# Optimization experiments

Hardware: AMD Instinct MI355X
Metric: run time of the kernel (lower is better)

Reference implementation:

```python
import jax, jax.numpy as jnp
import numpy as np
import math

NUM_HEADS = 16
ATTN_WIDTH = 256


def setup_inputs() -> dict:
    key = jax.random.key(0)
    ks = jax.random.split(key, 5)
    B, S, C, H = 2, 2048, 1024, 1024
    scale = 0.02
    return {
        "x": jax.random.normal(ks[0], (B, S, C), dtype=jnp.float32),
        "Wq": jax.random.normal(ks[1], (C, H), dtype=jnp.float32) * scale,
        "Wk": jax.random.normal(ks[2], (C, H), dtype=jnp.float32) * scale,
        "Wv": jax.random.normal(ks[3], (C, H), dtype=jnp.float32) * scale,
        "Wo": jax.random.normal(ks[4], (H, C), dtype=jnp.float32) * scale,
    }


def reference(x, Wq, Wk, Wv, Wo):
    B, S, C = x.shape
    H = NUM_HEADS
    dh = Wq.shape[1] // H  # head dim; Q.size(-1) in torch code

    def split_heads(t):
        # [B, S, H*dh] -> [B, H, S, dh]
        return t.reshape(B, S, H, dh).transpose(0, 2, 1, 3)

    q = split_heads(x @ Wq)
    k = split_heads(x @ Wk)
    v = split_heads(x @ Wv)

    scores = jnp.einsum("bhqd,bhkd->bhqk", q, k) / math.sqrt(dh)
    # exp-shift (first 'softmax-like' step, unnormalized)
    scores = jnp.exp(scores - jnp.max(scores, axis=-1, keepdims=True))
    # banded mask: tril(attn_width//2 - 1).triu(-(attn_width//2))
    i = jnp.arange(S)[:, None]
    j = jnp.arange(S)[None, :]
    d = j - i
    half = ATTN_WIDTH // 2
    mask = (d <= half - 1) & (d >= -half)
    scores = jnp.where(mask, scores, 0.0)
    # second softmax over the masked exp-scores (zeros contribute exp(0)=1)
    weights = jax.nn.softmax(scores, axis=-1)

    out = jnp.einsum("bhqk,bhkd->bhqd", weights, v)  # [B, H, S, dh]
    out = out.transpose(0, 2, 1, 3).reshape(B, S, H * dh)
    return out @ Wo
```

## Files before the change

kernel.cpp:

```cpp
#include <hip/hip_runtime.h>
#include <math.h>

typedef __bf16 bf16_t;
typedef bf16_t bf16x8 __attribute__((ext_vector_type(8)));
typedef bf16_t bf16x4 __attribute__((ext_vector_type(4)));
typedef float f32x4 __attribute__((ext_vector_type(4)));

constexpr int S_ = 2048;
constexpr float SCALE = 0.125f;

#define MFMA_B16(a, b, c) __builtin_amdgcn_mfma_f32_16x16x32_bf16(a, b, c, 0, 0, 0)

#define WAIT_VM0() __builtin_amdgcn_s_waitcnt(0x0F70)
#define WAIT_VM4() __builtin_amdgcn_s_waitcnt(0x0F74)
#define BARRIER()  __builtin_amdgcn_s_barrier()

typedef __attribute__((address_space(1))) const void* as1_cvp;
typedef __attribute__((address_space(3))) void* as3_vp;

__device__ __forceinline__ void gl2lds16(const void* g, void* l)
{
    __builtin_amdgcn_global_load_lds((as1_cvp)g, (as3_vp)l, 16, 0, 0);
}

#define SRC_SWZ8(lane) ((((lane) & 3) ^ (((lane) >> 3) & 3)) * 8)
#define RD_SWZ8(quad, l15) ((((quad) ^ (((l15) >> 1) & 3))) * 8)

__global__ __launch_bounds__(256) void prep(const float* __restrict__ x,
                                            const float* __restrict__ Wq,
                                            const float* __restrict__ Wk,
                                            const float* __restrict__ Wv,
                                            const float* __restrict__ Wo,
                                            bf16_t* __restrict__ xb,
                                            bf16_t* __restrict__ Wqt,
                                            bf16_t* __restrict__ Wkt,
                                            bf16_t* __restrict__ Wvt,
                                            bf16_t* __restrict__ Wot,
                                            float* __restrict__ vsp)
{
    __shared__ float T[64][65];
    const int blk = blockIdx.x;
    const int tid = threadIdx.x;
    if (blk < 1024) {
#pragma unroll
        for (int u = 0; u < 4; ++u) {
            const int g = blk * 1024 + u * 256 + tid;
            const float4 v = ((const float4*)x)[g];
            bf16x4 o;
            o[0] = (bf16_t)v.x; o[1] = (bf16_t)v.y;
            o[2] = (bf16_t)v.z; o[3] = (bf16_t)v.w;
            *(bf16x4*)&xb[(size_t)g * 4] = o;
        }
    } else if (blk < 2048) {
        const int rem = blk - 1024;
        const int wsel = rem >> 8, t = rem & 255;
        const float* src = (wsel == 0) ? Wq : (wsel == 1) ? Wk : (wsel == 2) ? Wv : Wo;
        bf16_t* dst = (wsel == 0) ? Wqt : (wsel == 1) ? Wkt : (wsel == 2) ? Wvt : Wot;
        const int k0 = (t >> 4) * 64, n0 = (t & 15) * 64;
        const int rr = tid >> 4, c4 = (tid & 15) * 4;
#pragma unroll
        for (int u = 0; u < 4; ++u) {
            const float4 v = *(const float4*)&src[(size_t)(k0 + u * 16 + rr) * 1024 + n0 + c4];
            T[u * 16 + rr][c4 + 0] = v.x; T[u * 16 + rr][c4 + 1] = v.y;
            T[u * 16 + rr][c4 + 2] = v.z; T[u * 16 + rr][c4 + 3] = v.w;
        }
        __syncthreads();
#pragma unroll
        for (int u = 0; u < 4; ++u) {
            bf16x4 o;
#pragma unroll
            for (int e = 0; e < 4; ++e) o[e] = (bf16_t)T[c4 + e][u * 16 + rr];
            *(bf16x4*)&dst[(size_t)(n0 + u * 16 + rr) * 1024 + k0 + c4] = o;
        }
    } else {
#pragma unroll
        for (int u = 0; u < 8; ++u) vsp[u * 256 + tid] = 0.f;
    }
}

template <int MODE>
__device__ __forceinline__ void mfma_gemm_body(bf16_t* __restrict__ As,
                                               bf16_t* __restrict__ Bs,
                                               const bf16_t* __restrict__ A,
                                               const bf16_t* __restrict__ Bt,
                                               void* __restrict__ dst,
                                               float* __restrict__ vsum_out,
                                               int m0, int n0)
{
    const int tid = threadIdx.x;
    const int lane = tid & 63, wid = tid >> 6;
    const int l15 = lane & 15, quad = lane >> 4;
    const int wm = (wid & 1) * 64, wn = (wid >> 1) * 64;

    const int srow = wid * 32 + (lane >> 2);
    const int scg8 = SRC_SWZ8(lane);
    const bf16_t* Ag0 = A  + (size_t)(m0 + srow) * 1024 + scg8;
    const bf16_t* Ag1 = A  + (size_t)(m0 + srow + 16) * 1024 + scg8;
    const bf16_t* Bg0 = Bt + (size_t)(n0 + srow) * 1024 + scg8;
    const bf16_t* Bg1 = Bt + (size_t)(n0 + srow + 16) * 1024 + scg8;

    const int rs = RD_SWZ8(quad, l15);

    f32x4 acc[4][4];
#pragma unroll
    for (int i = 0; i < 4; ++i)
#pragma unroll
        for (int j = 0; j < 4; ++j) acc[i][j] = (f32x4){0.f, 0.f, 0.f, 0.f};

#pragma unroll
    for (int p = 0; p < 2; ++p) {
        const int k0 = p * 32;
        gl2lds16(Ag0 + k0, As + p * 4096 + (wid * 2 + 0) * 512);
        gl2lds16(Ag1 + k0, As + p * 4096 + (wid * 2 + 1) * 512);
        gl2lds16(Bg0 + k0, Bs + p * 4096 + (wid * 2 + 0) * 512);
        gl2lds16(Bg1 + k0, Bs + p * 4096 + (wid * 2 + 1) * 512);
    }

#pragma unroll
    for (int it = 0; it < 32; ++it) {
        if (it < 30) WAIT_VM4(); else WAIT_VM0();
        BARRIER();
        if (it < 30) {
            const int k0 = (it + 2) * 32;
            const int sb = (it + 2) % 3;
            gl2lds16(Ag0 + k0, As + sb * 4096 + (wid * 2 + 0) * 512);
            gl2lds16(Ag1 + k0, As + sb * 4096 + (wid * 2 + 1) * 512);
            gl2lds16(Bg0 + k0, Bs + sb * 4096 + (wid * 2 + 0) * 512);
            gl2lds16(Bg1 + k0, Bs + sb * 4096 + (wid * 2 + 1) * 512);
        }
        const int cb = it % 3;
        bf16x8 af[4], bfr[4];
#pragma unroll
        for (int mt = 0; mt < 4; ++mt)
            af[mt] = *(const bf16x8*)&As[cb * 4096 + (wm + mt * 16 + l15) * 32 + rs];
#pragma unroll
        for (int nt = 0; nt < 4; ++nt)
            bfr[nt] = *(const bf16x8*)&Bs[cb * 4096 + (wn + nt * 16 + l15) * 32 + rs];
#pragma unroll
        for (int mt = 0; mt < 4; ++mt)
#pragma unroll
            for (int nt = 0; nt < 4; ++nt)
                acc[mt][nt] = MFMA_B16(bfr[nt], af[mt], acc[mt][nt]);
    }

#pragma unroll
    for (int mt = 0; mt < 4; ++mt) {
        const int m = m0 + wm + mt * 16 + l15;
#pragma unroll
        for (int nt = 0; nt < 4; ++nt) {
            const int nb = n0 + wn + nt * 16 + quad * 4;
            if (MODE == 0) {
                *(f32x4*)&((float*)dst)[(size_t)m * 1024 + nb] = acc[mt][nt];
            } else if (MODE == 1) {
                const int bb = m >> 11, s = m & 2047;
                const int hh = nb >> 6, d = nb & 63;
                bf16x4 o;
#pragma unroll
                for (int u = 0; u < 4; ++u) o[u] = (bf16_t)acc[mt][nt][u];
                *(bf16x4*)&((bf16_t*)dst)[((size_t)(bb * 16 + hh) * 2048 + s) * 64 + d] = o;
            } else {
                const int bb = n0 >> 11;
                const int hh = m >> 6, dd = m & 63;
                bf16x4 o;
#pragma unroll
                for (int u = 0; u < 4; ++u) o[u] = (bf16_t)acc[mt][nt][u];
                *(bf16x4*)&((bf16_t*)dst)[((size_t)(bb * 16 + hh) * 64 + dd) * 2048 + (nb & 2047)] = o;
            }
        }
    }

    if (MODE == 2 && vsum_out != nullptr) {
        const int bb = n0 >> 11;
#pragma unroll
        for (int mt = 0; mt < 4; ++mt) {
            float p = 0.f;
#pragma unroll
            for (int nt = 0; nt < 4; ++nt)
                p += acc[mt][nt][0] + acc[mt][nt][1] + acc[mt][nt][2] + acc[mt][nt][3];
            p += __shfl_xor(p, 16);
            p += __shfl_xor(p, 32);
            if (quad == 0) {
                const int m = m0 + wm + mt * 16 + l15;
                atomicAdd(&vsum_out[(bb * 16 + (m >> 6)) * 64 + (m & 63)], p);
            }
        }
    }
}

__device__ __forceinline__ int remap_m(void) { return (blockIdx.x << 2) + (blockIdx.y >> 3); }
__device__ __forceinline__ int remap_n(void) { return blockIdx.y & 7; }

__global__ __launch_bounds__(256) void gemm_qkv_mfma(const bf16_t* __restrict__ xb,
                                                     const bf16_t* __restrict__ Wqt,
                                                     const bf16_t* __restrict__ Wkt,
                                                     const bf16_t* __restrict__ Wvt,
                                                     bf16_t* Qh, bf16_t* Kh, bf16_t* VhT,
                                                     float* vsp)
{
    __shared__ bf16_t As[12288];
    __shared__ bf16_t Bs[12288];
    if (blockIdx.z == 2) {
        mfma_gemm_body<2>(As, Bs, Wvt, xb, VhT, vsp, remap_n() * 128, remap_m() * 128);
    } else {
        const bf16_t* Bt = (blockIdx.z == 0) ? Wqt : Wkt;
        bf16_t* dst = (blockIdx.z == 0) ? Qh : Kh;
        mfma_gemm_body<1>(As, Bs, xb, Bt, dst, nullptr, remap_m() * 128, remap_n() * 128);
    }
}

__global__ __launch_bounds__(256) void gemm_out_mfma(const bf16_t* __restrict__ attn,
                                                     const bf16_t* __restrict__ Wot,
                                                     float* __restrict__ out)
{
    __shared__ bf16_t As[12288];
    __shared__ bf16_t Bs[12288];
    mfma_gemm_body<0>(As, Bs, attn, Wot, out, nullptr, remap_m() * 128, remap_n() * 128);
}

__global__ __launch_bounds__(256) void attn_k(const bf16_t* __restrict__ Qh,
                                              const bf16_t* __restrict__ Kh,
                                              const bf16_t* __restrict__ VhT,
                                              const float* __restrict__ vsp,
                                              bf16_t* __restrict__ attn)
{
    __shared__ bf16_t Qs[8192];
    __shared__ float mr_sh[128];
    __shared__ __align__(16) char uni[18944];

    float*  msh = (float*)uni;
    bf16_t* Ws  = (bf16_t*)uni;
    float*  zsh = (float*)(uni + 18432);

    const int tid = threadIdx.x;
    const int lane = tid & 63, wid = tid >> 6;
    const int l15 = lane & 15, quad = lane >> 4;

    const int f = blockIdx.x;
    const int seq = f >> 3;
    const int bh = (f & 7) + 8 * (seq >> 4);
    const int i0 = (seq & 15) * 128;
    const int b = bh >> 4, h = bh & 15;
    const bf16_t* Qb  = Qh  + (size_t)bh * 131072;
    const bf16_t* Kb  = Kh  + (size_t)bh * 131072;
    const bf16_t* VbT = VhT + (size_t)bh * 131072;

    const int ssw = SRC_SWZ8(lane);
    const int rs  = RD_SWZ8(quad, l15);

#pragma unroll
    for (int c = 0; c < 4; ++c) {
        const int gg = wid * 4 + c;
        const int half = gg >> 3;
        const int row = (gg & 7) * 16 + (lane >> 2);
        gl2lds16(Qb + (size_t)(i0 + row) * 64 + half * 32 + ssw, Qs + gg * 512);
    }
    __syncthreads();

    bf16x8 af[8][2];
#pragma unroll
    for (int mt = 0; mt < 8; ++mt)
#pragma unroll
        for (int ks = 0; ks < 2; ++ks)
            af[mt][ks] = *(const bf16x8*)&Qs[ks * 4096 + (mt * 16 + l15) * 32 + rs];

    float vm[8];
#pragma unroll
    for (int mt = 0; mt < 8; ++mt) vm[mt] = -3.0e38f;

    const bf16_t* kf0 = Kb + (size_t)(wid * 16 + l15) * 64 + quad * 8;
    bf16x8 k0 = *(const bf16x8*)(kf0);
    bf16x8 k1 = *(const bf16x8*)(kf0 + 32);

    for (int jc = 0; jc < 32; ++jc) {
        const bf16_t* pn = kf0 + (size_t)((jc < 31) ? (jc + 1) : 31) * 4096;
        const bf16x8 n0 = *(const bf16x8*)(pn);
        const bf16x8 n1 = *(const bf16x8*)(pn + 32);
        __builtin_amdgcn_s_setprio(1);
#pragma unroll
        for (int mt = 0; mt < 8; ++mt) {
            f32x4 t = (f32x4){0.f, 0.f, 0.f, 0.f};
            t = MFMA_B16(k0, af[mt][0], t);
            t = MFMA_B16(k1, af[mt][1], t);
            const float u = fmaxf(fmaxf(t[0], t[1]), t[2]);
            vm[mt] = fmaxf(fmaxf(u, t[3]), vm[mt]);
        }
        __builtin_amdgcn_s_setprio(0);
        k0 = n0; k1 = n1;
    }

#pragma unroll
    for (int mt = 0; mt < 8; ++mt) {
        float v = vm[mt];
        v = fmaxf(v, __shfl_xor(v, 16));
        v = fmaxf(v, __shfl_xor(v, 32));
        if (quad == 0) msh[(wid * 8 + mt) * 16 + l15] = v;
    }
    __syncthreads();

    if (tid < 128) {
        const int mt = tid >> 4, il = tid & 15;
        const float v = fmaxf(fmaxf(msh[(0 * 8 + mt) * 16 + il], msh[(1 * 8 + mt) * 16 + il]),
                              fmaxf(msh[(2 * 8 + mt) * 16 + il], msh[(3 * 8 + mt) * 16 + il]));
        mr_sh[tid] = v * SCALE;
    }
    __syncthreads();

    bf16x8 aq[2][2];
#pragma unroll
    for (int t = 0; t < 2; ++t)
#pragma unroll
        for (int ks = 0; ks < 2; ++ks)
            aq[t][ks] = *(const bf16x8*)&Qs[ks * 4096 + ((wid * 2 + t) * 16 + l15) * 32 + rs];

    float mreg[2][4];
#pragma unroll
    for (int t = 0; t < 2; ++t)
#pragma unroll
        for (int r = 0; r < 4; ++r)
            mreg[t][r] = mr_sh[(wid * 2 + t) * 16 + quad * 4 + r];

    f32x4 vsd4[4];
#pragma unroll
    for (int dt = 0; dt < 4; ++dt)
        vsd4[dt] = *(const f32x4*)&vsp[bh * 64 + dt * 16 + quad * 4];

    f32x4 accO[2][4];
#pragma unroll
    for (int t = 0; t < 2; ++t)
#pragma unroll
        for (int dt = 0; dt < 4; ++dt) accO[t][dt] = (f32x4){0.f, 0.f, 0.f, 0.f};
    float zp[2][4] = {{0.f, 0.f, 0.f, 0.f}, {0.f, 0.f, 0.f, 0.f}};

    for (int cb2 = 0; cb2 < 6; ++cb2) {
        const int jb = i0 - 128 + cb2 * 64;
        if (jb < 0 || jb >= S_) continue;

#pragma unroll
        for (int t = 0; t < 2; ++t) {
            const int mt = wid * 2 + t;
#pragma unroll
            for (int jt4 = 0; jt4 < 4; ++jt4) {
                const bf16_t* kp = Kb + (size_t)(jb + jt4 * 16 + l15) * 64 + quad * 8;
                const bf16x8 kk0 = *(const bf16x8*)(kp);
                const bf16x8 kk1 = *(const bf16x8*)(kp + 32);
                f32x4 sc = (f32x4){0.f, 0.f, 0.f, 0.f};
                sc = MFMA_B16(aq[t][0], kk0, sc);
                sc = MFMA_B16(aq[t][1], kk1, sc);
#pragma unroll
                for (int r = 0; r < 4; ++r) {
                    const int ig = i0 + mt * 16 + quad * 4 + r;
                    const int jg = jb + jt4 * 16 + l15;
                    const int dd = jg - ig;
                    const bool ok = (dd >= -128) && (dd <= 127);
                    const float e1 = __expf(sc[r] * SCALE - mreg[t][r]);
                    const float wv = ok ? (__expf(e1) - 1.0f) : 0.0f;
                    const bf16_t wb = (bf16_t)wv;
                    zp[t][r] += (float)wb;
                    Ws[(mt * 16 + quad * 4 + r) * 72 + jt4 * 16 + l15] = wb;
                }
            }
        }

        __builtin_amdgcn_s_setprio(1);
#pragma unroll
        for (int ks = 0; ks < 2; ++ks) {
            bf16x8 bv[4];
#pragma unroll
            for (int dt = 0; dt < 4; ++dt)
                bv[dt] = *(const bf16x8*)(VbT + (size_t)(dt * 16 + l15) * 2048
                                          + jb + ks * 32 + quad * 8);
#pragma unroll
            for (int t = 0; t < 2; ++t) {
                const int mt = wid * 2 + t;
                const bf16x8 aw = *(const bf16x8*)&Ws[(mt * 16 + l15) * 72 + ks * 32 + quad * 8];
#pragma unroll
                for (int dt = 0; dt < 4; ++dt)
                    accO[t][dt] = MFMA_B16(bv[dt], aw, accO[t][dt]);
            }
        }
        __builtin_amdgcn_s_setprio(0);
    }

#pragma unroll
    for (int t = 0; t < 2; ++t)
#pragma unroll
        for (int r = 0; r < 4; ++r) {
            float z = zp[t][r];
            z += __shfl_xor(z, 1);
            z += __shfl_xor(z, 2);
            z += __shfl_xor(z, 4);
            z += __shfl_xor(z, 8);
            if (l15 == 0) zsh[wid * 32 + t * 16 + quad * 4 + r] = z + (float)S_;
        }
    __syncthreads();

#pragma unroll
    for (int t = 0; t < 2; ++t) {
        const float rz = 1.0f / zsh[wid * 32 + t * 16 + l15];
        const int irow = i0 + (wid * 2 + t) * 16 + l15;
#pragma unroll
        for (int dt = 0; dt < 4; ++dt) {
            bf16x4 o;
#pragma unroll
            for (int r = 0; r < 4; ++r)
                o[r] = (bf16_t)((accO[t][dt][r] + vsd4[dt][r]) * rz);
            *(bf16x4*)&attn[(size_t)(b * S_ + irow) * 1024 + h * 64 + dt * 16 + quad * 4] = o;
        }
    }
}

extern "C" void kernel_launch(void* const* d_in, const int* in_sizes, int n_in,
                              void* d_out, int out_size, void* d_ws, size_t ws_size,
                              hipStream_t stream)
{
    const float* x  = (const float*)d_in[0];
    const float* Wq = (const float*)d_in[1];
    const float* Wk = (const float*)d_in[2];
    const float* Wv = (const float*)d_in[3];
    const float* Wo = (const float*)d_in[4];
    float* out = (float*)d_out;

    char* ws = (char*)d_ws;
    bf16_t* xb   = (bf16_t*)(ws + 0);
    bf16_t* Wqt  = (bf16_t*)(ws + 8388608);
    bf16_t* Wkt  = (bf16_t*)(ws + 10485760);
    bf16_t* Wvt  = (bf16_t*)(ws + 12582912);
    bf16_t* Wot  = (bf16_t*)(ws + 14680064);
    bf16_t* Qh   = (bf16_t*)(ws + 16777216);
    bf16_t* Kh   = (bf16_t*)(ws + 25165824);
    bf16_t* VhT  = (bf16_t*)(ws + 33554432);
    bf16_t* attn = (bf16_t*)(ws + 41943040);
    float*  vsp  = (float*)(ws + 50331648);

    prep<<<2049, 256, 0, stream>>>(x, Wq, Wk, Wv, Wo, xb, Wqt, Wkt, Wvt, Wot, vsp);
    gemm_qkv_mfma<<<dim3(8, 32, 3), 256, 0, stream>>>(xb, Wqt, Wkt, Wvt, Qh, Kh, VhT, vsp);
    attn_k<<<512, 256, 0, stream>>>(Qh, Kh, VhT, vsp, attn);
    gemm_out_mfma<<<dim3(8, 32), 256, 0, stream>>>(attn, Wot, out);
}
```

Before: 189.9 us.

## Stage K and V^T tiles into double-buffered LDS via async global-to-LDS loads

The attention kernel now copies each 64-key chunk of K and V^T into swizzled, double-buffered LDS using global_load_lds, prefetching the next chunk while the current one is computed. The chunk range is also clamped up front instead of skipping out-of-range iterations. This replaces per-wave direct global loads, which every wave repeated for the same K/V data, with shared block-level staging. In exchange it raises LDS usage from about 19KB to about 52KB plus Q, which may lower occupancy, and it adds extra barriers per chunk and drops the setprio hints.

New measurement: 175.3 us. 7.7% less time.

```diff
diff --git a/kernel.cpp b/kernel.cpp
--- a/kernel.cpp
+++ b/kernel.cpp
@@ -225,11 +225,13 @@
 {
     __shared__ bf16_t Qs[8192];
     __shared__ float mr_sh[128];
-    __shared__ __align__(16) char uni[18944];
+    __shared__ __align__(16) char uni[51712];
 
     float*  msh = (float*)uni;
-    bf16_t* Ws  = (bf16_t*)uni;
-    float*  zsh = (float*)(uni + 18432);
+    bf16_t* Ks2 = (bf16_t*)uni;
+    bf16_t* VtL = (bf16_t*)(uni + 16384);
+    bf16_t* Ws  = (bf16_t*)(uni + 32768);
+    float*  zsh = (float*)(uni + 51200);
 
     const int tid = threadIdx.x;
     const int lane = tid & 63, wid = tid >> 6;
@@ -331,18 +333,52 @@
         for (int dt = 0; dt < 4; ++dt) accO[t][dt] = (f32x4){0.f, 0.f, 0.f, 0.f};
     float zp[2][4] = {{0.f, 0.f, 0.f, 0.f}, {0.f, 0.f, 0.f, 0.f}};
 
-    for (int cb2 = 0; cb2 < 6; ++cb2) {
-        const int jb = i0 - 128 + cb2 * 64;
-        if (jb < 0 || jb >= S_) continue;
+    const int jlo = (i0 - 128 < 0) ? 0 : (i0 - 128);
+    const int jhi = (i0 + 192 > S_ - 64) ? (S_ - 64) : (i0 + 192);
+    const int nc  = ((jhi - jlo) >> 6) + 1;
+
+#define STAGE_B(JB, SB)                                                          \
+    {                                                                            \
+        const int jb_ = (JB);                                                    \
+        const int sb_ = (SB);                                                    \
+        _Pragma("unroll")                                                        \
+        for (int c = 0; c < 2; ++c) {                                            \
+            const int gg = wid * 2 + c;                                          \
+            const int half = gg >> 2;                                            \
+            const int row = (gg & 3) * 16 + (lane >> 2);                         \
+            gl2lds16(Kb + (size_t)(jb_ + row) * 64 + half * 32 + ssw,            \
+                     Ks2 + sb_ * 4096 + gg * 512);                               \
+        }                                                                        \
+        _Pragma("unroll")                                                        \
+        for (int c = 0; c < 2; ++c) {                                            \
+            const int gg = wid * 2 + c;                                          \
+            const int d = gg * 8 + (lane >> 3);                                  \
+            const int jl = (lane & 7) ^ ((lane >> 3) & 7);                       \
+            gl2lds16(VbT + (size_t)d * 2048 + jb_ + jl * 8,                      \
+                     VtL + sb_ * 4096 + gg * 512);                               \
+        }                                                                        \
+    }
+
+    STAGE_B(jlo, 0);
+
+    for (int c = 0; c < nc; ++c) {
+        const int jb = jlo + c * 64;
+        const int cbuf = c & 1;
+        if (c + 1 < nc) {
+            STAGE_B(jlo + (c + 1) * 64, (c + 1) & 1);
+            WAIT_VM4();
+        } else {
+            WAIT_VM0();
+        }
+        BARRIER();
 
 #pragma unroll
         for (int t = 0; t < 2; ++t) {
             const int mt = wid * 2 + t;
 #pragma unroll
             for (int jt4 = 0; jt4 < 4; ++jt4) {
-                const bf16_t* kp = Kb + (size_t)(jb + jt4 * 16 + l15) * 64 + quad * 8;
-                const bf16x8 kk0 = *(const bf16x8*)(kp);
-                const bf16x8 kk1 = *(const bf16x8*)(kp + 32);
+                const bf16x8 kk0 = *(const bf16x8*)&Ks2[cbuf * 4096 + (jt4 * 16 + l15) * 32 + rs];
+                const bf16x8 kk1 = *(const bf16x8*)&Ks2[cbuf * 4096 + 2048 + (jt4 * 16 + l15) * 32 + rs];
                 f32x4 sc = (f32x4){0.f, 0.f, 0.f, 0.f};
                 sc = MFMA_B16(aq[t][0], kk0, sc);
                 sc = MFMA_B16(aq[t][1], kk1, sc);
@@ -360,15 +396,15 @@
                 }
             }
         }
-
-        __builtin_amdgcn_s_setprio(1);
+        __syncthreads();
+
 #pragma unroll
         for (int ks = 0; ks < 2; ++ks) {
             bf16x8 bv[4];
 #pragma unroll
             for (int dt = 0; dt < 4; ++dt)
-                bv[dt] = *(const bf16x8*)(VbT + (size_t)(dt * 16 + l15) * 2048
-                                          + jb + ks * 32 + quad * 8);
+                bv[dt] = *(const bf16x8*)&VtL[cbuf * 4096 + (dt * 16 + l15) * 64 +
+                                              (((ks * 4 + quad) ^ (l15 & 7)) * 8)];
 #pragma unroll
             for (int t = 0; t < 2; ++t) {
                 const int mt = wid * 2 + t;
@@ -378,8 +414,9 @@
                     accO[t][dt] = MFMA_B16(bv[dt], aw, accO[t][dt]);
             }
         }
-        __builtin_amdgcn_s_setprio(0);
-    }
+        __syncthreads();
+    }
+#undef STAGE_B
 
 #pragma unroll
     for (int t = 0; t < 2; ++t)
```
